# Performance work log

Hardware: AMD Instinct MI355X
Metric: run time of the kernel (lower is better)

Reference implementation:

```python
import jax, jax.numpy as jnp
import numpy as np

# --- hyperparameters (forward-arg constants, closed over) ---
NOShfS, NOShfR, NOShfA, NOShfZ = 16, 16, 8, 8
OEtaS, OEtaR, OEtaA, OZeta = 4.0, 4.0, 8.0, 8.0
LowerOShfS, UpperOShfS = -4.0, 4.0
LowerOShfR, UpperOShfR = 0.0, 2.0
LowerOShfA, UpperOShfA = 0.0, 2.0
LowerOShfZ, UpperOShfZ = 0.0, float(np.pi)

# --- per-species normalization tables (H row 0, O row 1) ---
H_MU = [-0.0013891633279463555, 0.052817133273316774, 0.139812833597163, 0.04197082575153015]
O_MU = [0.3869724094534165, 1.1195726605859562, 4.597656411500856, 4.18116756869605, -0.777753667038269, 0.8991094564592526, 0.25287442792706855]
H_SG = [0.014984132924379046, 0.06597323056314336, 0.05229082868259066, 0.10317217531939492]
O_SG = [0.01648580936203453, 0.04360467004470585, 0.10939958699162289, 0.1452881891452822, 0.24744978852384295, 0.6757096584771374, 0.15629951845443388]

def _pad(row, n, val):
    return row + [val] * (n - len(row))

S_MUS = np.array([_pad(H_MU, 9, 0.0), _pad(O_MU, 9, 0.0)], dtype=np.float32)
S_SGS = np.array([_pad(H_SG, 9, 1.0), _pad(O_SG, 9, 1.0)], dtype=np.float32)
D_REORDER = np.array([0, 2, 5, 4, 3, 1])


def setup_inputs() -> dict:
    key = jax.random.key(0)
    k1, k2 = jax.random.split(key)
    nconf, natoms = 128, 192
    coefficients = jax.random.normal(k1, (nconf, natoms, 45), dtype=jnp.float32)
    # atomic numbers: H (1) or O (8)
    species = jnp.where(jax.random.uniform(k2, (nconf, natoms)) < 0.5, 1, 8).astype(jnp.int32)
    return {"coefficients": coefficients, "species": species}


def reference(coefficients, species) -> jnp.ndarray:
    nconf, natoms, _ = coefficients.shape
    # _reshape_coefficients ('spd' path)
    s = coefficients[..., :9]                                   # [nc,na,9]
    p = coefficients[..., 9:21].reshape(nconf, natoms, 4, 3)    # [nc,na,4,3]
    d = coefficients[..., 21:].reshape(nconf, natoms, 4, 6)
    d = d[..., jnp.asarray(D_REORDER)]                          # xx,yy,zz,zy,zx,xy
    om = jnp.concatenate([p, d[..., :3], d[..., 3:]], axis=2)   # [nc,na,12,3] orbital matrix

    # s-coefficient normalization by species (H vs O)
    idx = (species == 8).astype(jnp.int32)
    mus = jnp.asarray(S_MUS)[idx]                               # [nc,na,9]
    sgs = jnp.asarray(S_SGS)[idx]
    s_n = (s - mus) / sgs

    OShfS = jnp.linspace(LowerOShfS, UpperOShfS, NOShfS, dtype=jnp.float32)
    s_aev = jnp.exp(-OEtaS * (s_n[..., None] - OShfS) ** 2)     # [nc,na,9,NOShfS]

    dist = jnp.linalg.norm(om, axis=-1)                         # [nc,na,12]
    OShfR = jnp.linspace(LowerOShfR, UpperOShfR, NOShfR, dtype=jnp.float32)
    r_aev = jnp.exp(-OEtaR * (dist[..., None] - OShfR) ** 2)    # [nc,na,12,NOShfR]

    # angles between all AOV pairs (i<j) -> 66 pairs
    zero_mask = jnp.all(jnp.abs(om) < 1e-12, axis=-1)           # [nc,na,12]
    safe_dist = jnp.where(zero_mask, 1.0, dist)
    u = jnp.where(zero_mask[..., None], 0.0, om / safe_dist[..., None])
    ii, jj = jnp.triu_indices(12, k=1)                          # row-major, matches the double loop
    cos_ang = jnp.einsum('cnad,cnad->cna', u[:, :, ii, :], u[:, :, jj, :])  # [nc,na,66]
    angles = jnp.arccos(0.9999 * cos_ang)
    avdist = (dist[:, :, ii] + dist[:, :, jj]) * 0.5            # [nc,na,66]

    OShfZ = jnp.linspace(LowerOShfZ, UpperOShfZ, NOShfZ, dtype=jnp.float32)
    OShfA = jnp.linspace(LowerOShfA, UpperOShfA, NOShfA, dtype=jnp.float32)
    f1 = ((1.0 + jnp.cos(angles[..., None] - OShfZ)) * 0.5) ** OZeta   # [nc,na,66,NOShfZ]
    f2 = jnp.exp(-OEtaA * (avdist[..., None] - OShfA) ** 2)            # [nc,na,66,NOShfA]
    ang_aev = (2.0 * f1[..., :, None] * f2[..., None, :]).reshape(nconf, natoms, -1)

    return jnp.concatenate([
        s_aev.reshape(nconf, natoms, -1),
        r_aev.reshape(nconf, natoms, -1),
        ang_aev,
    ], axis=-1)                                                 # [nc,na,4560]
```

## Files before the change

kernel.cpp:

```cpp
#include <hip/hip_runtime.h>

typedef float f32x4 __attribute__((ext_vector_type(4)));

__constant__ float c_mus[2][9] = {
  {-0.0013891633279463555f, 0.052817133273316774f, 0.139812833597163f, 0.04197082575153015f,
   0.f, 0.f, 0.f, 0.f, 0.f},
  {0.3869724094534165f, 1.1195726605859562f, 4.597656411500856f, 4.18116756869605f,
   -0.777753667038269f, 0.8991094564592526f, 0.25287442792706855f, 0.f, 0.f}
};
__constant__ float c_sgs[2][9] = {
  {0.014984132924379046f, 0.06597323056314336f, 0.05229082868259066f, 0.10317217531939492f,
   1.f, 1.f, 1.f, 1.f, 1.f},
  {0.01648580936203453f, 0.04360467004470585f, 0.10939958699162289f, 0.1452881891452822f,
   0.24744978852384295f, 0.6757096584771374f, 0.15629951845443388f, 1.f, 1.f}
};
__constant__ unsigned char c_ii[66] = {
  0,0,0,0,0,0,0,0,0,0,0,
  1,1,1,1,1,1,1,1,1,1,
  2,2,2,2,2,2,2,2,2,
  3,3,3,3,3,3,3,3,
  4,4,4,4,4,4,4,
  5,5,5,5,5,5,
  6,6,6,6,6,
  7,7,7,7,
  8,8,8,
  9,9,
  10
};
__constant__ unsigned char c_jj[66] = {
  1,2,3,4,5,6,7,8,9,10,11,
  2,3,4,5,6,7,8,9,10,11,
  3,4,5,6,7,8,9,10,11,
  4,5,6,7,8,9,10,11,
  5,6,7,8,9,10,11,
  6,7,8,9,10,11,
  7,8,9,10,11,
  8,9,10,11,
  9,10,11,
  10,11,
  11
};
__constant__ float c_cosZ[8] = {
  1.0f, 0.90096886790241915f, 0.62348980185873359f, 0.22252093395631439f,
  -0.22252093395631439f, -0.62348980185873359f, -0.90096886790241915f, -1.0f
};
__constant__ float c_sinZ[8] = {
  0.0f, 0.43388373911755823f, 0.78183148246802969f, 0.97492791218182362f,
  0.97492791218182362f, 0.78183148246802969f, 0.43388373911755823f, 0.0f
};

__global__ __launch_bounds__(256)
void aev_kernel(const float* __restrict__ coeff, const int* __restrict__ species,
                float* __restrict__ out, int ntotal) {
  const int A = blockIdx.x;
  if (A >= ntotal) return;
  const int tid = threadIdx.x;

  __shared__ float sh_coef[45];
  __shared__ float sh_sn[9];
  __shared__ float sh_dist[12];
  __shared__ float sh_u[12][3];
  __shared__ __align__(16) float sh_f1[66 * 8];
  __shared__ __align__(16) float sh_f2[66 * 8];

  if (tid < 45) sh_coef[tid] = coeff[(size_t)A * 45 + tid];
  __syncthreads();

  const int sidx = (species[A] == 8) ? 1 : 0;

  if (tid < 9) {
    sh_sn[tid] = (sh_coef[tid] - c_mus[sidx][tid]) / c_sgs[sidx][tid];
  } else if (tid >= 16 && tid < 28) {
    int k = tid - 16;
    float x, y, z;
    if (k < 4) {
      x = sh_coef[9 + 3 * k]; y = sh_coef[10 + 3 * k]; z = sh_coef[11 + 3 * k];
    } else if (k < 8) {
      int b = 21 + 6 * (k - 4);
      x = sh_coef[b + 0]; y = sh_coef[b + 2]; z = sh_coef[b + 5];
    } else {
      int b = 21 + 6 * (k - 8);
      x = sh_coef[b + 4]; y = sh_coef[b + 3]; z = sh_coef[b + 1];
    }
    float d = sqrtf(x * x + y * y + z * z);
    bool zero = (fabsf(x) < 1e-12f) && (fabsf(y) < 1e-12f) && (fabsf(z) < 1e-12f);
    float inv = zero ? 0.f : 1.f / d;
    sh_dist[k] = d;
    sh_u[k][0] = x * inv; sh_u[k][1] = y * inv; sh_u[k][2] = z * inv;
  }
  __syncthreads();

  if (tid < 66) {
    int i = c_ii[tid], j = c_jj[tid];
    float cosang = sh_u[i][0] * sh_u[j][0] + sh_u[i][1] * sh_u[j][1] + sh_u[i][2] * sh_u[j][2];
    float c = 0.9999f * cosang;
    float s = sqrtf(fmaxf(1.f - c * c, 0.f));
    float av = 0.5f * (sh_dist[i] + sh_dist[j]);
#pragma unroll
    for (int z = 0; z < 8; ++z) {
      float cz = c * c_cosZ[z] + s * c_sinZ[z];
      float b = (1.f + cz) * 0.5f;
      float b2 = b * b;
      float b4 = b2 * b2;
      sh_f1[tid * 8 + z] = 2.f * (b4 * b4);
      float da = av - (float)z * (2.f / 7.f);
      sh_f2[tid * 8 + z] = __expf(-8.f * da * da);
    }
  }
  __syncthreads();

  f32x4* out4 = (f32x4*)out + (size_t)A * 1140;

  {
    const int q = tid;
    const int i = q * 4;
    f32x4 v;
    if (i < 144) {
      int j = i >> 4, t = i & 15;
      float sn = sh_sn[j];
#pragma unroll
      for (int m = 0; m < 4; ++m) {
        float d = sn - (-4.f + (float)(t + m) * (8.f / 15.f));
        v[m] = __expf(-4.f * d * d);
      }
    } else if (i < 336) {
      int e = i - 144;
      int k = e >> 4, t = e & 15;
      float dd = sh_dist[k];
#pragma unroll
      for (int m = 0; m < 4; ++m) {
        float d = dd - (float)(t + m) * (2.f / 15.f);
        v[m] = __expf(-4.f * d * d);
      }
    } else {
      int e = i - 336;
      int p = e >> 6, z = (e >> 3) & 7, a = e & 7;
      float f1v = sh_f1[p * 8 + z];
      f32x4 f2v = *(const f32x4*)&sh_f2[p * 8 + a];
      v = f1v * f2v;
    }
    __builtin_nontemporal_store(v, &out4[q]);
  }

  {
    const int a  = (tid & 1) * 4;
    const int u0 = tid + 256 - 84;
    const int p0 = u0 >> 4;
    const int z0 = (u0 >> 1) & 7;
    const float* f1b = &sh_f1[p0 * 8 + z0];
    const float* f2b = &sh_f2[p0 * 8 + a];
    f32x4* ob = out4 + (tid + 256);
#pragma unroll
    for (int it = 0; it < 3; ++it) {
      float f1v = f1b[it * 128];
      f32x4 f2v = *(const f32x4*)&f2b[it * 128];
      f32x4 v = f1v * f2v;
      __builtin_nontemporal_store(v, &ob[it * 256]);
    }
    if (tid < 116) {
      float f1v = f1b[3 * 128];
      f32x4 f2v = *(const f32x4*)&f2b[3 * 128];
      f32x4 v = f1v * f2v;
      __builtin_nontemporal_store(v, &ob[3 * 256]);
    }
  }
}

extern "C" void kernel_launch(void* const* d_in, const int* in_sizes, int n_in,
                              void* d_out, int out_size, void* d_ws, size_t ws_size,
                              hipStream_t stream) {
  const float* coeff = (const float*)d_in[0];
  const int* species = (const int*)d_in[1];
  float* out = (float*)d_out;
  int ntotal = in_sizes[1];
  hipLaunchKernelGGL(aev_kernel, dim3(ntotal), dim3(256), 0, stream,
                     coeff, species, out, ntotal);
}
```

Measured before the change: 438.6 us.

## Process eight atoms per block to amortize setup and barriers

Each block now handles eight atoms instead of one. It computes the per-atom s-norms, distances, unit vectors and the f1/f2 tables for all eight with the full thread count, then streams the outputs of each atom in a loop. The aim is to cut per-block launch overhead, the three barriers per atom, and the idle threads during setup. In exchange there are fewer blocks (3072 instead of 24576) and more shared memory per block, which can lower occupancy and the number of stores in flight on a kernel that is bound by writes.

```diff
diff --git a/kernel.cpp b/kernel.cpp
--- a/kernel.cpp
+++ b/kernel.cpp
@@ -1,6 +1,8 @@
 #include <hip/hip_runtime.h>
 
 typedef float f32x4 __attribute__((ext_vector_type(4)));
+
+#define APB 8
 
 __constant__ float c_mus[2][9] = {
   {-0.0013891633279463555f, 0.052817133273316774f, 0.139812833597163f, 0.04197082575153015f,
@@ -52,116 +54,138 @@
 __global__ __launch_bounds__(256)
 void aev_kernel(const float* __restrict__ coeff, const int* __restrict__ species,
                 float* __restrict__ out, int ntotal) {
-  const int A = blockIdx.x;
-  if (A >= ntotal) return;
+  const int A0 = blockIdx.x * APB;
   const int tid = threadIdx.x;
 
-  __shared__ float sh_coef[45];
-  __shared__ float sh_sn[9];
-  __shared__ float sh_dist[12];
-  __shared__ float sh_u[12][3];
-  __shared__ __align__(16) float sh_f1[66 * 8];
-  __shared__ __align__(16) float sh_f2[66 * 8];
-
-  if (tid < 45) sh_coef[tid] = coeff[(size_t)A * 45 + tid];
-  __syncthreads();
-
-  const int sidx = (species[A] == 8) ? 1 : 0;
-
-  if (tid < 9) {
-    sh_sn[tid] = (sh_coef[tid] - c_mus[sidx][tid]) / c_sgs[sidx][tid];
-  } else if (tid >= 16 && tid < 28) {
-    int k = tid - 16;
-    float x, y, z;
-    if (k < 4) {
-      x = sh_coef[9 + 3 * k]; y = sh_coef[10 + 3 * k]; z = sh_coef[11 + 3 * k];
-    } else if (k < 8) {
-      int b = 21 + 6 * (k - 4);
-      x = sh_coef[b + 0]; y = sh_coef[b + 2]; z = sh_coef[b + 5];
-    } else {
-      int b = 21 + 6 * (k - 8);
-      x = sh_coef[b + 4]; y = sh_coef[b + 3]; z = sh_coef[b + 1];
-    }
-    float d = sqrtf(x * x + y * y + z * z);
-    bool zero = (fabsf(x) < 1e-12f) && (fabsf(y) < 1e-12f) && (fabsf(z) < 1e-12f);
-    float inv = zero ? 0.f : 1.f / d;
-    sh_dist[k] = d;
-    sh_u[k][0] = x * inv; sh_u[k][1] = y * inv; sh_u[k][2] = z * inv;
+  __shared__ float sh_sn[APB * 9];
+  __shared__ float sh_dist[APB * 12];
+  __shared__ float sh_u[APB * 12 * 3];
+  __shared__ __align__(16) float sh_f1[APB * 528];
+  __shared__ __align__(16) float sh_f2[APB * 528];
+
+  if (tid < APB * 9) {
+    int m = tid / 9, j = tid - 9 * m;
+    int A = A0 + m;
+    if (A < ntotal) {
+      int sidx = (species[A] == 8) ? 1 : 0;
+      float c = coeff[(size_t)A * 45 + j];
+      sh_sn[tid] = (c - c_mus[sidx][j]) / c_sgs[sidx][j];
+    }
+  } else if (tid >= 128 && tid < 128 + APB * 12) {
+    int w = tid - 128;
+    int m = w / 12, k = w - 12 * m;
+    int A = A0 + m;
+    if (A < ntotal) {
+      const float* cb = coeff + (size_t)A * 45;
+      float x, y, z;
+      if (k < 4) {
+        x = cb[9 + 3 * k]; y = cb[10 + 3 * k]; z = cb[11 + 3 * k];
+      } else if (k < 8) {
+        const float* b = cb + 21 + 6 * (k - 4);
+        x = b[0]; y = b[2]; z = b[5];
+      } else {
+        const float* b = cb + 21 + 6 * (k - 8);
+        x = b[4]; y = b[3]; z = b[1];
+      }
+      float d = sqrtf(x * x + y * y + z * z);
+      bool zero = (fabsf(x) < 1e-12f) && (fabsf(y) < 1e-12f) && (fabsf(z) < 1e-12f);
+      float inv = zero ? 0.f : 1.f / d;
+      sh_dist[w] = d;
+      sh_u[w * 3 + 0] = x * inv; sh_u[w * 3 + 1] = y * inv; sh_u[w * 3 + 2] = z * inv;
+    }
   }
   __syncthreads();
 
-  if (tid < 66) {
-    int i = c_ii[tid], j = c_jj[tid];
-    float cosang = sh_u[i][0] * sh_u[j][0] + sh_u[i][1] * sh_u[j][1] + sh_u[i][2] * sh_u[j][2];
-    float c = 0.9999f * cosang;
-    float s = sqrtf(fmaxf(1.f - c * c, 0.f));
-    float av = 0.5f * (sh_dist[i] + sh_dist[j]);
-#pragma unroll
-    for (int z = 0; z < 8; ++z) {
-      float cz = c * c_cosZ[z] + s * c_sinZ[z];
-      float b = (1.f + cz) * 0.5f;
-      float b2 = b * b;
-      float b4 = b2 * b2;
-      sh_f1[tid * 8 + z] = 2.f * (b4 * b4);
-      float da = av - (float)z * (2.f / 7.f);
-      sh_f2[tid * 8 + z] = __expf(-8.f * da * da);
+#pragma unroll
+  for (int rep = 0; rep < 3; ++rep) {
+    int h = tid + rep * 256;
+    if (h < APB * 66) {
+      int m = h / 66, pr = h - 66 * m;
+      int i = c_ii[pr], j = c_jj[pr];
+      const float* ui = &sh_u[(m * 12 + i) * 3];
+      const float* uj = &sh_u[(m * 12 + j) * 3];
+      float cosang = ui[0] * uj[0] + ui[1] * uj[1] + ui[2] * uj[2];
+      float c = 0.9999f * cosang;
+      float s = sqrtf(fmaxf(1.f - c * c, 0.f));
+      float av = 0.5f * (sh_dist[m * 12 + i] + sh_dist[m * 12 + j]);
+      float* f1p = &sh_f1[m * 528 + pr * 8];
+      float* f2p = &sh_f2[m * 528 + pr * 8];
+#pragma unroll
+      for (int zh = 0; zh < 2; ++zh) {
+        f32x4 v1, v2;
+#pragma unroll
+        for (int q = 0; q < 4; ++q) {
+          int z = zh * 4 + q;
+          float cz = c * c_cosZ[z] + s * c_sinZ[z];
+          float b = (1.f + cz) * 0.5f;
+          float b2 = b * b;
+          float b4 = b2 * b2;
+          v1[q] = 2.f * (b4 * b4);
+          float da = av - (float)z * (2.f / 7.f);
+          v2[q] = __expf(-8.f * da * da);
+        }
+        *(f32x4*)(f1p + zh * 4) = v1;
+        *(f32x4*)(f2p + zh * 4) = v2;
+      }
     }
   }
   __syncthreads();
 
-  f32x4* out4 = (f32x4*)out + (size_t)A * 1140;
-
-  {
-    const int q = tid;
-    const int i = q * 4;
-    f32x4 v;
-    if (i < 144) {
-      int j = i >> 4, t = i & 15;
-      float sn = sh_sn[j];
-#pragma unroll
-      for (int m = 0; m < 4; ++m) {
-        float d = sn - (-4.f + (float)(t + m) * (8.f / 15.f));
-        v[m] = __expf(-4.f * d * d);
+  const int i0 = tid * 4;
+  const int a4 = (tid & 1) * 4;
+  const int u0 = tid + 172;
+  const int offA = u0 >> 1;
+  const int offB = ((u0 >> 4) << 3) + a4;
+
+  f32x4* outg = (f32x4*)out;
+  for (int m = 0; m < APB; ++m) {
+    int A = A0 + m;
+    if (A >= ntotal) break;
+    f32x4* out4 = outg + (size_t)A * 1140;
+    const float* f1a = &sh_f1[m * 528];
+    const float* f2a = &sh_f2[m * 528];
+    const float* snm = &sh_sn[m * 9];
+    const float* dm  = &sh_dist[m * 12];
+    {
+      f32x4 v;
+      if (i0 < 144) {
+        int j = i0 >> 4, t = i0 & 15;
+        float sn = snm[j];
+#pragma unroll
+        for (int q = 0; q < 4; ++q) {
+          float d = sn - (-4.f + (float)(t + q) * (8.f / 15.f));
+          v[q] = __expf(-4.f * d * d);
+        }
+      } else if (i0 < 336) {
+        int e = i0 - 144;
+        int k = e >> 4, t = e & 15;
+        float dd = dm[k];
+#pragma unroll
+        for (int q = 0; q < 4; ++q) {
+          float d = dd - (float)(t + q) * (2.f / 15.f);
+          v[q] = __expf(-4.f * d * d);
+        }
+      } else {
+        int e = i0 - 336;
+        int p = e >> 6, z = (e >> 3) & 7, a = e & 7;
+        float f1v = f1a[p * 8 + z];
+        f32x4 f2v = *(const f32x4*)&f2a[p * 8 + a];
+        v = f1v * f2v;
       }
-    } else if (i < 336) {
-      int e = i - 144;
-      int k = e >> 4, t = e & 15;
-      float dd = sh_dist[k];
-#pragma unroll
-      for (int m = 0; m < 4; ++m) {
-        float d = dd - (float)(t + m) * (2.f / 15.f);
-        v[m] = __expf(-4.f * d * d);
-      }
-    } else {
-      int e = i - 336;
-      int p = e >> 6, z = (e >> 3) & 7, a = e & 7;
-      float f1v = sh_f1[p * 8 + z];
-      f32x4 f2v = *(const f32x4*)&sh_f2[p * 8 + a];
-      v = f1v * f2v;
-    }
-    __builtin_nontemporal_store(v, &out4[q]);
-  }
-
-  {
-    const int a  = (tid & 1) * 4;
-    const int u0 = tid + 256 - 84;
-    const int p0 = u0 >> 4;
-    const int z0 = (u0 >> 1) & 7;
-    const float* f1b = &sh_f1[p0 * 8 + z0];
-    const float* f2b = &sh_f2[p0 * 8 + a];
-    f32x4* ob = out4 + (tid + 256);
+      __builtin_nontemporal_store(v, &out4[tid]);
+    }
 #pragma unroll
     for (int it = 0; it < 3; ++it) {
-      float f1v = f1b[it * 128];
-      f32x4 f2v = *(const f32x4*)&f2b[it * 128];
+      float f1v = f1a[offA + it * 128];
+      f32x4 f2v = *(const f32x4*)&f2a[offB + it * 128];
       f32x4 v = f1v * f2v;
-      __builtin_nontemporal_store(v, &ob[it * 256]);
+      __builtin_nontemporal_store(v, &out4[tid + 256 + it * 256]);
     }
     if (tid < 116) {
-      float f1v = f1b[3 * 128];
-      f32x4 f2v = *(const f32x4*)&f2b[3 * 128];
+      float f1v = f1a[offA + 384];
+      f32x4 f2v = *(const f32x4*)&f2a[offB + 384];
       f32x4 v = f1v * f2v;
-      __builtin_nontemporal_store(v, &ob[3 * 256]);
+      __builtin_nontemporal_store(v, &out4[tid + 1024]);
     }
   }
 }
@@ -173,6 +197,7 @@
   const int* species = (const int*)d_in[1];
   float* out = (float*)d_out;
   int ntotal = in_sizes[1];
-  hipLaunchKernelGGL(aev_kernel, dim3(ntotal), dim3(256), 0, stream,
+  int nblocks = (ntotal + APB - 1) / APB;
+  hipLaunchKernelGGL(aev_kernel, dim3(nblocks), dim3(256), 0, stream,
                      coeff, species, out, ntotal);
 }
```

Result: slower. 451.6 us (+3.0%).
